# Optimization experiments

Hardware: AMD Instinct MI355X
Metric: run time of the kernel (lower is better)

Reference implementation:

```python
import jax, jax.numpy as jnp
import numpy as np

B = 32768
P = 32  # max_poles == max_zeros
NC = P + 1  # count classes 0..32
BIG = 1e30

POLE_COUNT_W = 5.0
ZERO_COUNT_W = 5.0
POLE_VALUE_W = 1.0
ZERO_VALUE_W = 1.0


def setup_inputs() -> dict:
    key = jax.random.key(0)
    ks = jax.random.split(key, 8)
    return {
        "pole_count_logits": jax.random.normal(ks[0], (B, NC), jnp.float32),
        "zero_count_logits": jax.random.normal(ks[1], (B, NC), jnp.float32),
        "poles_all": jax.random.normal(ks[2], (B, P, 2), jnp.float32),
        "zeros_all": jax.random.normal(ks[3], (B, P, 2), jnp.float32),
        "target_poles_pad": jax.random.normal(ks[4], (B, P, 2), jnp.float32),
        "target_zeros_pad": jax.random.normal(ks[5], (B, P, 2), jnp.float32),
        "target_num_poles": jax.random.randint(ks[6], (B,), 0, NC, jnp.int32),
        "target_num_zeros": jax.random.randint(ks[7], (B,), 0, NC, jnp.int32),
    }


def _cross_entropy(logits, targets):
    logp = jax.nn.log_softmax(logits, axis=-1)
    nll = -jnp.take_along_axis(logp, targets[:, None].astype(jnp.int32), axis=1)[:, 0]
    return jnp.mean(nll)


def _masked_chamfer(pred, tgt, n_pred, n_tgt):
    """Vectorized variable-length chamfer. pred/tgt: [B,P,2], counts: [B]."""
    ar = jnp.arange(pred.shape[1])
    pm = ar[None, :] < n_pred[:, None]  # [B,P] valid pred mask
    tm = ar[None, :] < n_tgt[:, None]   # [B,P] valid target mask
    diff = pred[:, :, None, :] - tgt[:, None, :, :]  # [B,P,T,2]
    d = jnp.sum(diff * diff, axis=-1)                # [B,P,T] |z_p - z_t|^2
    min_p2t = jnp.min(jnp.where(tm[:, None, :], d, BIG), axis=2)  # [B,P]
    mean_p2t = jnp.sum(jnp.where(pm, min_p2t, 0.0), axis=1) / jnp.maximum(n_pred, 1).astype(pred.dtype)
    min_t2p = jnp.min(jnp.where(pm[:, :, None], d, BIG), axis=1)  # [B,T]
    mean_t2p = jnp.sum(jnp.where(tm, min_t2p, 0.0), axis=1) / jnp.maximum(n_tgt, 1).astype(pred.dtype)
    both = mean_p2t + mean_t2p
    sum_tgt_sq = jnp.sum(jnp.where(tm[:, :, None], tgt * tgt, 0.0), axis=(1, 2))
    sum_pred_sq = jnp.sum(jnp.where(pm[:, :, None], pred * pred, 0.0), axis=(1, 2))
    p0 = n_pred == 0
    t0 = n_tgt == 0
    out = jnp.where(p0 & t0, 0.0,
          jnp.where(p0, sum_tgt_sq,
          jnp.where(t0, sum_pred_sq, both)))
    return out  # [B]


def reference(pole_count_logits, zero_count_logits, poles_all, zeros_all,
              target_poles_pad, target_zeros_pad, target_num_poles, target_num_zeros):
    loss_pole_count = _cross_entropy(pole_count_logits, target_num_poles)
    loss_zero_count = _cross_entropy(zero_count_logits, target_num_zeros)

    pred_pole_counts = jnp.argmax(pole_count_logits, axis=-1).astype(jnp.int32)
    pred_zero_counts = jnp.argmax(zero_count_logits, axis=-1).astype(jnp.int32)

    pole_losses = _masked_chamfer(poles_all, target_poles_pad, pred_pole_counts, target_num_poles)
    zero_losses = _masked_chamfer(zeros_all, target_zeros_pad, pred_zero_counts, target_num_zeros)
    loss_pole_value = jnp.mean(pole_losses)
    loss_zero_value = jnp.mean(zero_losses)

    total_loss = (POLE_COUNT_W * loss_pole_count + ZERO_COUNT_W * loss_zero_count
                  + POLE_VALUE_W * loss_pole_value + ZERO_VALUE_W * loss_zero_value)
    return total_loss
```

## Files before the change

### kernel.cpp

```cpp
#include <hip/hip_runtime.h>
#include <float.h>

#define NCNT 33
#define NPTS 32

typedef float f32x2 __attribute__((ext_vector_type(2)));

__device__ __forceinline__ f32x2 mk2(float a, float b) { f32x2 r; r.x = a; r.y = b; return r; }

template<int CTRL, bool BC>
__device__ __forceinline__ int dpp_i(int old, int v) {
    return __builtin_amdgcn_update_dpp(old, v, CTRL, 0xF, 0xF, BC);
}

__device__ __forceinline__ float wave_sum63(float v) {
    v += __int_as_float(dpp_i<0x111, true>(0, __float_as_int(v)));
    v += __int_as_float(dpp_i<0x112, true>(0, __float_as_int(v)));
    v += __int_as_float(dpp_i<0x114, true>(0, __float_as_int(v)));
    v += __int_as_float(dpp_i<0x118, true>(0, __float_as_int(v)));
    v += __int_as_float(dpp_i<0x142, true>(0, __float_as_int(v)));
    v += __int_as_float(dpp_i<0x143, true>(0, __float_as_int(v)));
    return __int_as_float(__builtin_amdgcn_readlane(__float_as_int(v), 63));
}

__device__ __forceinline__ float wave_max63(float v) {
#define MX_STEP(C)                                                                    \
    {                                                                                 \
        int o = dpp_i<C, false>(__float_as_int(v), __float_as_int(v));                \
        v = fmaxf(v, __int_as_float(o));                                              \
    }
    MX_STEP(0x111) MX_STEP(0x112) MX_STEP(0x114) MX_STEP(0x118) MX_STEP(0x142) MX_STEP(0x143)
#undef MX_STEP
    return __int_as_float(__builtin_amdgcn_readlane(__float_as_int(v), 63));
}

__global__ __launch_bounds__(64) void vltf_kernel(
    const float* __restrict__ pole_logits, const float* __restrict__ zero_logits,
    const float* __restrict__ poles_all,   const float* __restrict__ zeros_all,
    const float* __restrict__ tpoles,      const float* __restrict__ tzeros,
    const int* __restrict__ tnum_p,        const int* __restrict__ tnum_z,
    float* __restrict__ partials)
{
    __shared__ __align__(16) float myl[192];

    const int lane = threadIdx.x;
    const int unit = blockIdx.x;
    const int row  = unit >> 1;
    const int part = unit & 1;

    const float* logits = part ? zero_logits : pole_logits;
    const float* predp  = part ? zeros_all   : poles_all;
    const float* tgtp   = part ? tzeros      : tpoles;
    const int*   tnum   = part ? tnum_z      : tnum_p;

    float x = (lane < NCNT) ? logits[row * NCNT + lane] : -FLT_MAX;
    float vmax = wave_max63(x);
    unsigned long long bm = __ballot(lane < NCNT && x == vmax);
    const int np = (int)__builtin_ctzll(bm);
    float e = (lane < NCNT) ? __expf(x - vmax) : 0.f;
    float sume = wave_sum63(e);
    const int nt = tnum[row];
    float xt = __int_as_float(__builtin_amdgcn_readlane(__float_as_int(x), nt));
    float nll = vmax + __logf(sume) - xt;

    const bool isPred = lane < 32;
    const int  idx    = lane & 31;
    const float2* ownArr = (const float2*)(isPred ? predp : tgtp);
    const float2  Pt     = ownArr[row * NPTS + idx];
    const int  nown = isPred ? np : nt;
    const bool vown = idx < nown;
    const float sreal = fmaf(Pt.x, Pt.x, Pt.y * Pt.y);

    const int wbase = isPred ? 96 : 0;
    const int uvpos = wbase + ((idx >> 1) << 2) + (idx & 1);
    myl[uvpos]            = vown ? -2.f * Pt.x : 0.f;
    myl[uvpos + 2]        = vown ? -2.f * Pt.y : 0.f;
    myl[wbase + 64 + idx] = vown ? sreal : 1e30f;
    __syncthreads();

    const int rbase = isPred ? 0 : 96;
    const float4* UVo = (const float4*)(myl + rbase);
    const float4* So  = (const float4*)(myl + rbase + 64);
    const f32x2 Pxv = mk2(Pt.x, Pt.x);
    const f32x2 Pyv = mk2(Pt.y, Pt.y);
    float m = FLT_MAX;
#pragma unroll
    for (int i = 0; i < 8; ++i) {
        float4 uv0 = UVo[2 * i], uv1 = UVo[2 * i + 1];
        float4 s4  = So[i];
        f32x2 val0 = Pyv * mk2(uv0.z, uv0.w) + mk2(s4.x, s4.y);
        val0       = Pxv * mk2(uv0.x, uv0.y) + val0;
        f32x2 val1 = Pyv * mk2(uv1.z, uv1.w) + mk2(s4.z, s4.w);
        val1       = Pxv * mk2(uv1.x, uv1.y) + val1;
        m = fminf(m, fminf(val0.x, val0.y));
        m = fminf(m, fminf(val1.x, val1.y));
    }

    float T;
    if (np > 0 && nt > 0) {
        float inv_n = __builtin_amdgcn_rcpf((float)nown);
        T = vown ? (m + sreal) * inv_n : 0.f;
    } else if (np == 0 && nt == 0) {
        T = 0.f;
    } else if (np == 0) {
        T = (!isPred && vown) ? sreal : 0.f;
    } else {
        T = (isPred && vown) ? sreal : 0.f;
    }
    float cham = wave_sum63(T);

    if (lane == 0) partials[unit] = 5.f * nll + cham;
}

__global__ __launch_bounds__(1024) void vltf_finalize(
    const float4* __restrict__ p4, int n4, float invB, float* __restrict__ out)
{
    float s = 0.f;
    for (int i = threadIdx.x; i < n4; i += 1024) {
        float4 v = p4[i];
        s += (v.x + v.y) + (v.z + v.w);
    }
    s = wave_sum63(s);
    __shared__ float sh[16];
    if ((threadIdx.x & 63) == 0) sh[threadIdx.x >> 6] = s;
    __syncthreads();
    if (threadIdx.x == 0) {
        float t = 0.f;
#pragma unroll
        for (int i = 0; i < 16; ++i) t += sh[i];
        out[0] = t * invB;
    }
}

extern "C" void kernel_launch(void* const* d_in, const int* in_sizes, int n_in,
                              void* d_out, int out_size, void* d_ws, size_t ws_size,
                              hipStream_t stream) {
    const float* pole_logits = (const float*)d_in[0];
    const float* zero_logits = (const float*)d_in[1];
    const float* poles_all   = (const float*)d_in[2];
    const float* zeros_all   = (const float*)d_in[3];
    const float* tpoles      = (const float*)d_in[4];
    const float* tzeros      = (const float*)d_in[5];
    const int*   tnp         = (const int*)d_in[6];
    const int*   tnz         = (const int*)d_in[7];

    const int B     = in_sizes[6];
    const int units = 2 * B;

    float* partials = (float*)d_ws;

    vltf_kernel<<<units, 64, 0, stream>>>(pole_logits, zero_logits,
                                          poles_all, zeros_all,
                                          tpoles, tzeros, tnp, tnz, partials);
    vltf_finalize<<<1, 1024, 0, stream>>>((const float4*)partials, units / 4,
                                          1.0f / (float)B, (float*)d_out);
}
```

Baseline: 108.7 us.

## Replace LDS all-pairs staging with register DPP rotations and pack four waves per block

The kernel no longer stages the opposite point set in shared memory behind a barrier. Each half-wave now swaps its partner set in registers with a cross-half shuffle, then walks all 32 pairs using row-rotate DPP steps plus one ds_swizzle that exchanges the 16-lane halves. The launch also packs four independent wave-units into each 256-thread block, so far fewer tiny blocks are dispatched. This removes LDS traffic and the barrier, but adds roughly 93 DPP moves and loses the packed two-wide FMA math of the old loop.

```diff
diff --git a/kernel.cpp b/kernel.cpp
--- a/kernel.cpp
+++ b/kernel.cpp
@@ -3,10 +3,6 @@
 
 #define NCNT 33
 #define NPTS 32
-
-typedef float f32x2 __attribute__((ext_vector_type(2)));
-
-__device__ __forceinline__ f32x2 mk2(float a, float b) { f32x2 r; r.x = a; r.y = b; return r; }
 
 template<int CTRL, bool BC>
 __device__ __forceinline__ int dpp_i(int old, int v) {
@@ -34,17 +30,24 @@
     return __int_as_float(__builtin_amdgcn_readlane(__float_as_int(v), 63));
 }
 
-__global__ __launch_bounds__(64) void vltf_kernel(
+__device__ __forceinline__ float rot_ror1(float v) {
+    return __int_as_float(dpp_i<0x121, false>(__float_as_int(v), __float_as_int(v)));
+}
+
+__device__ __forceinline__ float swz_x16(float v) {
+    return __int_as_float(__builtin_amdgcn_ds_swizzle(__float_as_int(v), 0x401F));
+}
+
+__global__ __launch_bounds__(256) void vltf_kernel(
     const float* __restrict__ pole_logits, const float* __restrict__ zero_logits,
     const float* __restrict__ poles_all,   const float* __restrict__ zeros_all,
     const float* __restrict__ tpoles,      const float* __restrict__ tzeros,
     const int* __restrict__ tnum_p,        const int* __restrict__ tnum_z,
-    float* __restrict__ partials)
+    float* __restrict__ partials, int units)
 {
-    __shared__ __align__(16) float myl[192];
-
-    const int lane = threadIdx.x;
-    const int unit = blockIdx.x;
+    const int lane = threadIdx.x & 63;
+    const int unit = (blockIdx.x << 2) | (threadIdx.x >> 6);
+    if (unit >= units) return;
     const int row  = unit >> 1;
     const int part = unit & 1;
 
@@ -71,30 +74,29 @@
     const bool vown = idx < nown;
     const float sreal = fmaf(Pt.x, Pt.x, Pt.y * Pt.y);
 
-    const int wbase = isPred ? 96 : 0;
-    const int uvpos = wbase + ((idx >> 1) << 2) + (idx & 1);
-    myl[uvpos]            = vown ? -2.f * Pt.x : 0.f;
-    myl[uvpos + 2]        = vown ? -2.f * Pt.y : 0.f;
-    myl[wbase + 64 + idx] = vown ? sreal : 1e30f;
-    __syncthreads();
+    float su = vown ? -2.f * Pt.x : 0.f;
+    float sv = vown ? -2.f * Pt.y : 0.f;
+    float ss = vown ? sreal       : 1e30f;
 
-    const int rbase = isPred ? 0 : 96;
-    const float4* UVo = (const float4*)(myl + rbase);
-    const float4* So  = (const float4*)(myl + rbase + 64);
-    const f32x2 Pxv = mk2(Pt.x, Pt.x);
-    const f32x2 Pyv = mk2(Pt.y, Pt.y);
-    float m = FLT_MAX;
+    float ou = __shfl_xor(su, 32);
+    float ov = __shfl_xor(sv, 32);
+    float os = __shfl_xor(ss, 32);
+
+    float m0 = FLT_MAX, m1 = FLT_MAX;
 #pragma unroll
-    for (int i = 0; i < 8; ++i) {
-        float4 uv0 = UVo[2 * i], uv1 = UVo[2 * i + 1];
-        float4 s4  = So[i];
-        f32x2 val0 = Pyv * mk2(uv0.z, uv0.w) + mk2(s4.x, s4.y);
-        val0       = Pxv * mk2(uv0.x, uv0.y) + val0;
-        f32x2 val1 = Pyv * mk2(uv1.z, uv1.w) + mk2(s4.z, s4.w);
-        val1       = Pxv * mk2(uv1.x, uv1.y) + val1;
-        m = fminf(m, fminf(val0.x, val0.y));
-        m = fminf(m, fminf(val1.x, val1.y));
+    for (int t = 0; t < 16; ++t) {
+        float val = fmaf(Pt.x, ou, fmaf(Pt.y, ov, os));
+        if (t & 1) m1 = fminf(m1, val); else m0 = fminf(m0, val);
+        if (t < 15) { ou = rot_ror1(ou); ov = rot_ror1(ov); os = rot_ror1(os); }
     }
+    ou = swz_x16(ou); ov = swz_x16(ov); os = swz_x16(os);
+#pragma unroll
+    for (int t = 0; t < 16; ++t) {
+        float val = fmaf(Pt.x, ou, fmaf(Pt.y, ov, os));
+        if (t & 1) m1 = fminf(m1, val); else m0 = fminf(m0, val);
+        if (t < 15) { ou = rot_ror1(ou); ov = rot_ror1(ov); os = rot_ror1(os); }
+    }
+    float m = fminf(m0, m1);
 
     float T;
     if (np > 0 && nt > 0) {
@@ -149,9 +151,11 @@
 
     float* partials = (float*)d_ws;
 
-    vltf_kernel<<<units, 64, 0, stream>>>(pole_logits, zero_logits,
-                                          poles_all, zeros_all,
-                                          tpoles, tzeros, tnp, tnz, partials);
+    const int blocks = (units + 3) / 4;
+    vltf_kernel<<<blocks, 256, 0, stream>>>(pole_logits, zero_logits,
+                                            poles_all, zeros_all,
+                                            tpoles, tzeros, tnp, tnz,
+                                            partials, units);
     vltf_finalize<<<1, 1024, 0, stream>>>((const float4*)partials, units / 4,
                                           1.0f / (float)B, (float*)d_out);
 }
```

Measured after the change: 130.8 us. 1.2x slower.
